# Kernel optimization log

Measured on AMD Instinct MI355X. Metric: run time of the kernel, lower is better.

## Reference

```python
import jax, jax.numpy as jnp
import numpy as np

T = 4096   # total prefill tokens
HK = 16    # local_num_k_heads
HV = 16    # local_num_v_heads
DK = 128   # head_k_dim
DV = 128   # head_v_dim
KW = 4     # linear_conv_kernel_dim
QKV = HK * DK * 2 + HV * DV  # 6144


def setup_inputs() -> dict:
    key = jax.random.key(0)
    ks = jax.random.split(key, 6)
    return {
        "mixed_qkv": jax.random.normal(ks[0], (T, QKV), jnp.float32),
        "forget_gate": jax.random.normal(ks[1], (T, HV * DK), jnp.float32),
        "beta": jax.random.normal(ks[2], (T, HV), jnp.float32),
        "conv_weights": jax.random.normal(ks[3], (QKV, KW), jnp.float32) * 0.1,
        "A_log": jax.random.normal(ks[4], (HV,), jnp.float32),
        "dt_bias": jax.random.normal(ks[5], (HV, DK), jnp.float32),
    }


def _causal_conv1d_silu(x, w):
    # x: [T, C], w: [C, K] depthwise causal conv (no bias) + SiLU, matching causal_conv1d_fn
    C = x.shape[1]
    xt = x.T[None]                       # [1, C, T]
    y = jax.lax.conv_general_dilated(
        xt, w[:, None, :], window_strides=(1,), padding=[(KW - 1, 0)],
        feature_group_count=C)           # [1, C, T]
    return jax.nn.silu(y[0].T)           # [T, C]


def _l2norm(x, eps=1e-6):
    return x * jax.lax.rsqrt(jnp.sum(x * x, axis=-1, keepdims=True) + eps)


def reference(mixed_qkv, forget_gate, beta, conv_weights, A_log, dt_bias):
    # 1) depthwise causal conv1d + silu over packed qkv
    qkv = _causal_conv1d_silu(mixed_qkv, conv_weights)
    q, k, v = jnp.split(qkv, [HK * DK, 2 * HK * DK], axis=-1)
    # use_qk_l2norm_in_kernel=True; scale=None -> DK**-0.5 applied to q
    q = _l2norm(q.reshape(T, HK, DK)) * (DK ** -0.5)
    k = _l2norm(k.reshape(T, HK, DK))
    v = v.reshape(T, HV, DV)
    # use_gate_in_kernel=True (fused_kda_gate): g = -exp(A_log) * softplus(g_raw + dt_bias)
    g = -jnp.exp(A_log)[None, :, None] * jax.nn.softplus(
        forget_gate.reshape(T, HV, DK) + dt_bias[None])      # [T, H, DK] (log-decay)
    b = jax.nn.sigmoid(beta.astype(jnp.float32))             # [T, H]

    # 2) gated delta-rule recurrence (KDA), state S: [H, DK, DV]
    def step(S, inp):
        qt, kt, vt, gt, bt = inp
        S = S * jnp.exp(gt)[:, :, None]                      # per-dim forget
        pred = jnp.einsum('hk,hkv->hv', kt, S)               # memory readout
        delta = bt[:, None] * (vt - pred)                    # delta rule
        S = S + kt[:, :, None] * delta[:, None, :]
        o = jnp.einsum('hk,hkv->hv', qt, S)
        return S, o

    S0 = jnp.zeros((HV, DK, DV), jnp.float32)  # no prior ssm cache (fresh prefill)
    _, out = jax.lax.scan(step, S0, (q, k, v, g, b))
    return out  # [T, H, DV]
```

## Files before the change

kernel.cpp:

```cpp
#include <hip/hip_runtime.h>
#include <math.h>

#define TT   4096
#define HH   16
#define DK   128
#define QKV  6144
#define NQ   2048
#define KW   4

#define CK      16
#define NCHUNK  256
#define CG      2
#define NCG     64

#define ROTADD(x, r) x += __int_as_float(__builtin_amdgcn_update_dpp( \
    0, __float_as_int(x), 0x120 + (r), 0xf, 0xf, true))

#define XHALF(x) x += __int_as_float(__builtin_amdgcn_ds_swizzle( \
    __float_as_int(x), 0x401F))

#define COMP(a, i) ((i&3)==0 ? a[(i)>>2].x : (i&3)==1 ? a[(i)>>2].y \
                  : (i&3)==2 ? a[(i)>>2].z : a[(i)>>2].w)

#define ASYNC16(glb, lds) __builtin_amdgcn_global_load_lds( \
    (const __attribute__((address_space(1))) unsigned int*)(glb), \
    (__attribute__((address_space(3))) unsigned int*)(lds), 16, 0, 0)

#define WAIT_LGKM0 do { asm volatile("s_waitcnt lgkmcnt(0)" ::: "memory"); \
    __builtin_amdgcn_sched_barrier(0); } while(0)
#define WAIT_VM(N) do { asm volatile("s_waitcnt vmcnt(" #N ")" ::: "memory"); \
    __builtin_amdgcn_sched_barrier(0); } while(0)

__global__ __launch_bounds__(256) void kda_prep(
    const float* __restrict__ x,
    const float* __restrict__ fg,
    const float* __restrict__ cw,
    const float* __restrict__ A_log,
    const float* __restrict__ dtb,
    float* __restrict__ qn,
    float* __restrict__ kn,
    float* __restrict__ gout,
    float* __restrict__ vout)
{
    __shared__ float buf[QKV];
    const int t   = blockIdx.x;
    const int tid = threadIdx.x;

    for (int c = tid; c < QKV; c += 256) {
        const float4 w = *(const float4*)(cw + (size_t)c * 4);
        float acc = 0.f;
        if (t >= 3) {
            acc = x[(size_t)(t-3)*QKV + c]*w.x + x[(size_t)(t-2)*QKV + c]*w.y
                + x[(size_t)(t-1)*QKV + c]*w.z + x[(size_t)t*QKV + c]*w.w;
        } else {
            if (t-3 >= 0) acc += x[(size_t)(t-3)*QKV + c] * w.x;
            if (t-2 >= 0) acc += x[(size_t)(t-2)*QKV + c] * w.y;
            if (t-1 >= 0) acc += x[(size_t)(t-1)*QKV + c] * w.z;
            acc += x[(size_t)t*QKV + c] * w.w;
        }
        buf[c] = acc / (1.f + expf(-acc));
    }
    __syncthreads();

    {
        const int grp = tid >> 3;
        const int l8  = tid & 7;
        const float* src = buf + grp*DK + l8*16;
        float vals[16];
        float ss = 0.f;
        #pragma unroll
        for (int i = 0; i < 16; ++i) { vals[i] = src[i]; ss += vals[i]*vals[i]; }
        ss += __shfl_xor(ss, 1);
        ss += __shfl_xor(ss, 2);
        ss += __shfl_xor(ss, 4);
        float scale = 1.0f / sqrtf(ss + 1e-6f);
        const bool isq = (grp < 16);
        if (isq) scale *= 0.08838834764831845f;
        float* dst = (isq ? (qn + (size_t)t*NQ + grp*DK)
                          : (kn + (size_t)t*NQ + (grp-16)*DK)) + l8*16;
        #pragma unroll
        for (int i = 0; i < 16; ++i) dst[i] = vals[i]*scale;
    }

    for (int c = tid; c < NQ; c += 256)
        vout[(size_t)t*NQ + c] = buf[4096 + c];

    for (int c = tid; c < NQ; c += 256) {
        const int hh = c >> 7;
        const float xx = fg[(size_t)t*NQ + c] + dtb[c];
        const float sp = fmaxf(xx, 0.f) + log1pf(expf(-fabsf(xx)));
        gout[(size_t)t*NQ + c] = -expf(A_log[hh]) * sp;
    }
}

__global__ __launch_bounds__(256) void kda_chunkpre(
    float* __restrict__ Ab, float* __restrict__ Bb, float* __restrict__ Cb,
    const float* __restrict__ beta,
    float* __restrict__ GL, float* __restrict__ Qm,
    const float* __restrict__ vin,
    float* __restrict__ vt)
{
    __shared__ float gc_s[CK][DK+1];
    __shared__ float kb[CK][DK+1];
    __shared__ float qb[CK][DK+1];
    __shared__ float ktil[CK][DK+1];
    __shared__ float vb[CK][DK+1];
    __shared__ float pmat[CK][CK];
    __shared__ float xmat[CK][CK];
    __shared__ float bvals[CK];
    const int chunk = blockIdx.x, h = blockIdx.y, tid = threadIdx.x;
    const size_t base = ((size_t)chunk*CK)*NQ + h*DK;

    if (tid < CK) {
        const float bb = beta[(size_t)(chunk*CK + tid)*HH + h];
        bvals[tid] = 1.f / (1.f + expf(-bb));
    }
    if (tid < DK) {
        const int k = tid;
        float gc[CK], kv[CK], qv[CK];
        float run = 0.f;
        #pragma unroll
        for (int j = 0; j < CK; ++j) {
            run += Cb[base + (size_t)j*NQ + k];
            gc[j] = run;
            kv[j] = Bb[base + (size_t)j*NQ + k];
            qv[j] = Ab[base + (size_t)j*NQ + k];
            gc_s[j][k] = run; kb[j][k] = kv[j]; qb[j][k] = qv[j];
        }
        const float gL = gc[CK-1];
        GL[((size_t)chunk*HH + h)*DK + k] = expf(gL);
        #pragma unroll
        for (int j = 0; j < CK; ++j) {
            const float e = expf(gc[j]);
            Ab[base + (size_t)j*NQ + k] = qv[j]*e;
            ktil[j][k] = kv[j]*e;
            Cb[base + (size_t)j*NQ + k] = kv[j]*expf(gL - gc[j]);
        }
    }
    for (int idx = tid; idx < CK*DK; idx += 256)
        vb[idx>>7][idx&127] =
            vin[(size_t)(chunk*CK + (idx>>7))*NQ + h*DK + (idx&127)];

    if (tid < CK*CK) xmat[tid>>4][tid&15] = 0.f;
    __syncthreads();

    const size_t mqbase = ((size_t)chunk*HH + h)*(CK*CK);
    if (tid < 136) {
        int j = 0, i = tid;
        while (i > j) { i -= (j+1); ++j; }
        float accp = 0.f, accq = 0.f;
        #pragma unroll 4
        for (int k = 0; k < DK; ++k) {
            const float e = __expf(gc_s[j][k] - gc_s[i][k]);
            const float kie = kb[i][k]*e;
            accq = fmaf(qb[j][k], kie, accq);
            accp = fmaf(kb[j][k], kie, accp);
        }
        Qm[mqbase + j*CK + i] = accq;
        if (j > i) pmat[j][i] = accp;
    } else {
        int a = 1, u = tid - 136;
        while (u >= a) { u -= a; ++a; }
        Qm[mqbase + u*CK + a] = 0.f;
    }
    __syncthreads();

    if (tid < CK) {
        const int i = tid;
        for (int j = i; j < CK; ++j) {
            float s = (j == i) ? 1.f : 0.f;
            for (int m = i; m < j; ++m) s -= pmat[j][m]*xmat[m][i];
            xmat[j][i] = bvals[j]*s;
        }
    }
    __syncthreads();

    for (int idx = tid; idx < CK*DK; idx += 256) {
        const int j = idx >> 7, k2 = idx & 127;
        float aE = 0.f, aV = 0.f;
        #pragma unroll
        for (int m = 0; m < CK; ++m) {
            const float xm = xmat[j][m];
            aE = fmaf(xm, ktil[m][k2], aE);
            aV = fmaf(xm, vb[m][k2], aV);
        }
        Bb[base + (size_t)j*NQ + k2] = aE;
        vt[(size_t)(chunk*CK + j)*NQ + h*DK + k2] = aV;
    }
}

__global__ __launch_bounds__(64) void kda_scan(
    const float* __restrict__ Em,
    const float* __restrict__ qS,
    const float* __restrict__ wm,
    const float* __restrict__ GL,
    const float* __restrict__ Qm,
    const float* __restrict__ vin,
    float* __restrict__ vo)
{
    __shared__ __attribute__((aligned(16))) float s_e[CK][DK];
    __shared__ __attribute__((aligned(16))) float s_q[CK][DK];
    __shared__ __attribute__((aligned(16))) float s_w[2][CK][DK];
    __shared__ __attribute__((aligned(16))) float s_g[2][DK];
    __shared__ __attribute__((aligned(16))) float s_v[CK][4];

    const int tid   = threadIdx.x;
    const int ks    = tid & 15;
    const int half  = (tid >> 4) & 1;
    const int col   = tid >> 5;
    const int h     = blockIdx.x;
    const int cgoff = blockIdx.y * CG;
    const int hoff  = h * DK;
    const int r0    = half*64 + ks*4;
    const int vcol  = (cgoff & 3) + col;

    float4 S = {0,0,0,0};
    float4 pfQ[4], Qr[4];

#define STAGE_EQV(CC) do { \
    const size_t rb_ = (size_t)(CC)*CK; \
    _Pragma("unroll") \
    for (int r_ = 0; r_ < 8; ++r_) { \
        const int f_ = tid + r_*64;                   \
        const int j_ = f_ >> 5, c4_ = f_ & 31; \
        const size_t go_ = (rb_ + j_)*NQ + hoff + c4_*4; \
        ASYNC16(Em + go_, &s_e[0][0] + f_*4); \
        ASYNC16(qS + go_, &s_q[0][0] + f_*4); \
    } \
    if (tid < 16)                                     \
        ASYNC16(vin + (rb_ + tid)*NQ + hoff + (cgoff & ~3), \
                &s_v[0][0] + tid*4); \
} while(0)

#define STAGE_WGQ(CC, BB) do { \
    const size_t rb_ = (size_t)(CC)*CK; \
    _Pragma("unroll") \
    for (int r_ = 0; r_ < 8; ++r_) { \
        const int f_ = tid + r_*64; \
        const int j_ = f_ >> 5, c4_ = f_ & 31; \
        ASYNC16(wm + (rb_ + j_)*NQ + hoff + c4_*4, &s_w[BB][0][0] + f_*4); \
    } \
    if (tid < 32)                                     \
        ASYNC16(GL + ((size_t)(CC)*HH + h)*DK + tid*4, &s_g[BB][0] + tid*4); \
    { const size_t mb_ = ((size_t)(CC)*HH + h)*256 + ks*16; \
      _Pragma("unroll") \
      for (int r_ = 0; r_ < 4; ++r_) \
          pfQ[r_] = *(const float4*)(Qm + mb_ + r_*4); } \
} while(0)

    STAGE_WGQ(0, 0);
    STAGE_EQV(0);
    WAIT_VM(0);
    #pragma unroll
    for (int r = 0; r < 4; ++r) Qr[r] = pfQ[r];

    for (int c = 0; c < NCHUNK; ++c) {
        const int p = c & 1;
        const bool more = (c + 1 < NCHUNK);
        if (more) STAGE_WGQ(c + 1, 1 - p);

        float u[CK];
        float myo0 = 0.f;
        #pragma unroll
        for (int j = 0; j < CK; ++j) {
            const float4 Ea = *(const float4*)&s_e[j][r0];
            const float4 qa = *(const float4*)&s_q[j][r0];
            float pp = Ea.x*S.x;
            pp = fmaf(Ea.y, S.y, pp); pp = fmaf(Ea.z, S.z, pp); pp = fmaf(Ea.w, S.w, pp);
            float oo = qa.x*S.x;
            oo = fmaf(qa.y, S.y, oo); oo = fmaf(qa.z, S.z, oo); oo = fmaf(qa.w, S.w, oo);
            ROTADD(pp, 8); ROTADD(pp, 4); ROTADD(pp, 2); ROTADD(pp, 1);
            ROTADD(oo, 8); ROTADD(oo, 4); ROTADD(oo, 2); ROTADD(oo, 1);
            XHALF(pp);
            XHALF(oo);
            u[j] = s_v[j][vcol] - pp;
            myo0 = (j == ks) ? oo : myo0;
        }

        WAIT_LGKM0;
        if (more) STAGE_EQV(c + 1);

        const float4 ga = *(const float4*)&s_g[p][r0];
        S.x *= ga.x; S.y *= ga.y; S.z *= ga.z; S.w *= ga.w;

        float oacc = 0.f;
        #pragma unroll
        for (int i = 0; i < CK; ++i) {
            const float ui = u[i];
            const float4 wa = *(const float4*)&s_w[p][i][r0];
            S.x = fmaf(wa.x, ui, S.x); S.y = fmaf(wa.y, ui, S.y);
            S.z = fmaf(wa.z, ui, S.z); S.w = fmaf(wa.w, ui, S.w);
            oacc = fmaf(COMP(Qr, i), ui, oacc);
        }
        if (half == 0)
            vo[((size_t)(c*CK + ks))*NQ + hoff + cgoff + col] = myo0 + oacc;

        if (more) {
            #pragma unroll
            for (int r = 0; r < 4; ++r) Qr[r] = pfQ[r];
            WAIT_VM(1);
        }
    }
#undef STAGE_EQV
#undef STAGE_WGQ
}

extern "C" void kernel_launch(void* const* d_in, const int* in_sizes, int n_in,
                              void* d_out, int out_size, void* d_ws, size_t ws_size,
                              hipStream_t stream) {
    const float* x     = (const float*)d_in[0];
    const float* fg    = (const float*)d_in[1];
    const float* beta  = (const float*)d_in[2];
    const float* cw    = (const float*)d_in[3];
    const float* A_log = (const float*)d_in[4];
    const float* dtb   = (const float*)d_in[5];
    float* out = (float*)d_out;
    float* ws  = (float*)d_ws;

    const size_t TN = (size_t)TT * NQ;
    float* A_  = ws;
    float* B_  = ws + TN;
    float* C_  = ws + 2*TN;

    float* scratch = (float*)d_in[1];
    float* GLp = scratch;
    float* Qm  = scratch + (size_t)524288;

    float* vtil = (float*)d_in[0];

    hipLaunchKernelGGL(kda_prep, dim3(TT), dim3(256), 0, stream,
                       x, fg, cw, A_log, dtb, A_, B_, C_, out);
    hipLaunchKernelGGL(kda_chunkpre, dim3(NCHUNK, HH), dim3(256), 0, stream,
                       A_, B_, C_, beta, GLp, Qm, out, vtil);
    hipLaunchKernelGGL(kda_scan, dim3(HH, NCG), dim3(64), 0, stream,
                       B_, A_, C_, GLp, Qm, vtil, out);
}
```

Before: 921.4 us.

## Give each scan thread 8 state rows and 4 value columns per block

The scan kernel is rebalanced so each lane holds two float4 slices of state (rows r and r+64) instead of one. This removes the cross-half swizzle reduction and the idle half of the lanes at output time, and each 64-lane block now covers 4 value columns instead of 2, halving the grid. The cost is more registers and LDS reads per lane on the serial chunk loop, and only half as many blocks are available to fill the GPU.

New measurement: 1.073 ms. +16.5%, slower.

```diff
diff --git a/kernel.cpp b/kernel.cpp
--- a/kernel.cpp
+++ b/kernel.cpp
@@ -10,14 +10,11 @@
 
 #define CK      16
 #define NCHUNK  256
-#define CG      2
-#define NCG     64
+#define CG      4
+#define NCG     32
 
 #define ROTADD(x, r) x += __int_as_float(__builtin_amdgcn_update_dpp( \
     0, __float_as_int(x), 0x120 + (r), 0xf, 0xf, true))
-
-#define XHALF(x) x += __int_as_float(__builtin_amdgcn_ds_swizzle( \
-    __float_as_int(x), 0x401F))
 
 #define COMP(a, i) ((i&3)==0 ? a[(i)>>2].x : (i&3)==1 ? a[(i)>>2].y \
                   : (i&3)==2 ? a[(i)>>2].z : a[(i)>>2].w)
@@ -202,19 +199,17 @@
     __shared__ __attribute__((aligned(16))) float s_q[CK][DK];
     __shared__ __attribute__((aligned(16))) float s_w[2][CK][DK];
     __shared__ __attribute__((aligned(16))) float s_g[2][DK];
-    __shared__ __attribute__((aligned(16))) float s_v[CK][4];
+    __shared__ __attribute__((aligned(16))) float s_v[CK][CG];
 
     const int tid   = threadIdx.x;
     const int ks    = tid & 15;
-    const int half  = (tid >> 4) & 1;
-    const int col   = tid >> 5;
+    const int col   = tid >> 4;
     const int h     = blockIdx.x;
     const int cgoff = blockIdx.y * CG;
     const int hoff  = h * DK;
-    const int r0    = half*64 + ks*4;
-    const int vcol  = (cgoff & 3) + col;
-
-    float4 S = {0,0,0,0};
+    const int r1 = ks*4, r2 = 64 + ks*4;
+
+    float4 S1 = {0,0,0,0}, S2 = {0,0,0,0};
     float4 pfQ[4], Qr[4];
 
 #define STAGE_EQV(CC) do { \
@@ -228,8 +223,7 @@
         ASYNC16(qS + go_, &s_q[0][0] + f_*4); \
     } \
     if (tid < 16)                                     \
-        ASYNC16(vin + (rb_ + tid)*NQ + hoff + (cgoff & ~3), \
-                &s_v[0][0] + tid*4); \
+        ASYNC16(vin + (rb_ + tid)*NQ + hoff + cgoff, &s_v[0][0] + tid*4); \
 } while(0)
 
 #define STAGE_WGQ(CC, BB) do { \
@@ -263,37 +257,47 @@
         float myo0 = 0.f;
         #pragma unroll
         for (int j = 0; j < CK; ++j) {
-            const float4 Ea = *(const float4*)&s_e[j][r0];
-            const float4 qa = *(const float4*)&s_q[j][r0];
-            float pp = Ea.x*S.x;
-            pp = fmaf(Ea.y, S.y, pp); pp = fmaf(Ea.z, S.z, pp); pp = fmaf(Ea.w, S.w, pp);
-            float oo = qa.x*S.x;
-            oo = fmaf(qa.y, S.y, oo); oo = fmaf(qa.z, S.z, oo); oo = fmaf(qa.w, S.w, oo);
+            const float4 Ea  = *(const float4*)&s_e[j][r1];
+            const float4 Eb  = *(const float4*)&s_e[j][r2];
+            const float4 qa  = *(const float4*)&s_q[j][r1];
+            const float4 qb4 = *(const float4*)&s_q[j][r2];
+            float pa = Ea.x*S1.x;
+            pa = fmaf(Ea.y, S1.y, pa); pa = fmaf(Ea.z, S1.z, pa); pa = fmaf(Ea.w, S1.w, pa);
+            float pb = Eb.x*S2.x;
+            pb = fmaf(Eb.y, S2.y, pb); pb = fmaf(Eb.z, S2.z, pb); pb = fmaf(Eb.w, S2.w, pb);
+            float pp = pa + pb;
+            float oa = qa.x*S1.x;
+            oa = fmaf(qa.y, S1.y, oa); oa = fmaf(qa.z, S1.z, oa); oa = fmaf(qa.w, S1.w, oa);
+            float ob = qb4.x*S2.x;
+            ob = fmaf(qb4.y, S2.y, ob); ob = fmaf(qb4.z, S2.z, ob); ob = fmaf(qb4.w, S2.w, ob);
+            float oo = oa + ob;
             ROTADD(pp, 8); ROTADD(pp, 4); ROTADD(pp, 2); ROTADD(pp, 1);
             ROTADD(oo, 8); ROTADD(oo, 4); ROTADD(oo, 2); ROTADD(oo, 1);
-            XHALF(pp);
-            XHALF(oo);
-            u[j] = s_v[j][vcol] - pp;
+            u[j] = s_v[j][col] - pp;
             myo0 = (j == ks) ? oo : myo0;
         }
 
         WAIT_LGKM0;
         if (more) STAGE_EQV(c + 1);
 
-        const float4 ga = *(const float4*)&s_g[p][r0];
-        S.x *= ga.x; S.y *= ga.y; S.z *= ga.z; S.w *= ga.w;
+        const float4 ga = *(const float4*)&s_g[p][r1];
+        const float4 gb = *(const float4*)&s_g[p][r2];
+        S1.x *= ga.x; S1.y *= ga.y; S1.z *= ga.z; S1.w *= ga.w;
+        S2.x *= gb.x; S2.y *= gb.y; S2.z *= gb.z; S2.w *= gb.w;
 
         float oacc = 0.f;
         #pragma unroll
         for (int i = 0; i < CK; ++i) {
             const float ui = u[i];
-            const float4 wa = *(const float4*)&s_w[p][i][r0];
-            S.x = fmaf(wa.x, ui, S.x); S.y = fmaf(wa.y, ui, S.y);
-            S.z = fmaf(wa.z, ui, S.z); S.w = fmaf(wa.w, ui, S.w);
+            const float4 wa = *(const float4*)&s_w[p][i][r1];
+            const float4 wb = *(const float4*)&s_w[p][i][r2];
+            S1.x = fmaf(wa.x, ui, S1.x); S1.y = fmaf(wa.y, ui, S1.y);
+            S1.z = fmaf(wa.z, ui, S1.z); S1.w = fmaf(wa.w, ui, S1.w);
+            S2.x = fmaf(wb.x, ui, S2.x); S2.y = fmaf(wb.y, ui, S2.y);
+            S2.z = fmaf(wb.z, ui, S2.z); S2.w = fmaf(wb.w, ui, S2.w);
             oacc = fmaf(COMP(Qr, i), ui, oacc);
         }
-        if (half == 0)
-            vo[((size_t)(c*CK + ks))*NQ + hoff + cgoff + col] = myo0 + oacc;
+        vo[((size_t)(c*CK + ks))*NQ + hoff + cgoff + col] = myo0 + oacc;
 
         if (more) {
             #pragma unroll
```

## Restructure scan LDS staging: cache E in registers, double-buffer q/v, use permlane32 swap

Applied to the files above, without the earlier changes.

Reorganizes the per-chunk staging in the recurrence scan. E rows are copied into registers so the E buffer can be refilled early. q, v and g are double-buffered and prefetched a chunk ahead, while w is single-buffered and refilled after its last use. The thread mapping swaps the half/col roles so the cross-half reduction can use permlane32_swap instead of ds_swizzle. The hand-tuned vmcnt wait counts are fragile and must match the exact number of issued async loads, and the register-cached E copy raises register pressure.

Result: slower. 961.4 us (+4.3%).

```diff
diff --git a/kernel.cpp b/kernel.cpp
--- a/kernel.cpp
+++ b/kernel.cpp
@@ -16,8 +16,11 @@
 #define ROTADD(x, r) x += __int_as_float(__builtin_amdgcn_update_dpp( \
     0, __float_as_int(x), 0x120 + (r), 0xf, 0xf, true))
 
-#define XHALF(x) x += __int_as_float(__builtin_amdgcn_ds_swizzle( \
-    __float_as_int(x), 0x401F))
+typedef int int2v __attribute__((ext_vector_type(2)));
+#define XH32(x) do { \
+    int2v r_ = __builtin_amdgcn_permlane32_swap( \
+        __float_as_int(x), __float_as_int(x), false, false); \
+    x = __int_as_float(r_[0]) + __int_as_float(r_[1]); } while(0)
 
 #define COMP(a, i) ((i&3)==0 ? a[(i)>>2].x : (i&3)==1 ? a[(i)>>2].y \
                   : (i&3)==2 ? a[(i)>>2].z : a[(i)>>2].w)
@@ -199,15 +202,15 @@
     float* __restrict__ vo)
 {
     __shared__ __attribute__((aligned(16))) float s_e[CK][DK];
-    __shared__ __attribute__((aligned(16))) float s_q[CK][DK];
-    __shared__ __attribute__((aligned(16))) float s_w[2][CK][DK];
+    __shared__ __attribute__((aligned(16))) float s_q[2][CK][DK];
+    __shared__ __attribute__((aligned(16))) float s_w[CK][DK];
     __shared__ __attribute__((aligned(16))) float s_g[2][DK];
-    __shared__ __attribute__((aligned(16))) float s_v[CK][4];
+    __shared__ __attribute__((aligned(16))) float s_v[2][CK][4];
 
     const int tid   = threadIdx.x;
     const int ks    = tid & 15;
-    const int half  = (tid >> 4) & 1;
-    const int col   = tid >> 5;
+    const int col   = (tid >> 4) & 1;
+    const int half  = tid >> 5;
     const int h     = blockIdx.x;
     const int cgoff = blockIdx.y * CG;
     const int hoff  = h * DK;
@@ -215,31 +218,19 @@
     const int vcol  = (cgoff & 3) + col;
 
     float4 S = {0,0,0,0};
-    float4 pfQ[4], Qr[4];
-
-#define STAGE_EQV(CC) do { \
+    float4 pfQ[4], Qr[4], eR[CK];
+
+#define STAGE_QVG(CC, BB) do { \
     const size_t rb_ = (size_t)(CC)*CK; \
     _Pragma("unroll") \
     for (int r_ = 0; r_ < 8; ++r_) { \
         const int f_ = tid + r_*64;                   \
         const int j_ = f_ >> 5, c4_ = f_ & 31; \
-        const size_t go_ = (rb_ + j_)*NQ + hoff + c4_*4; \
-        ASYNC16(Em + go_, &s_e[0][0] + f_*4); \
-        ASYNC16(qS + go_, &s_q[0][0] + f_*4); \
+        ASYNC16(qS + (rb_ + j_)*NQ + hoff + c4_*4, &s_q[BB][0][0] + f_*4); \
     } \
     if (tid < 16)                                     \
         ASYNC16(vin + (rb_ + tid)*NQ + hoff + (cgoff & ~3), \
-                &s_v[0][0] + tid*4); \
-} while(0)
-
-#define STAGE_WGQ(CC, BB) do { \
-    const size_t rb_ = (size_t)(CC)*CK; \
-    _Pragma("unroll") \
-    for (int r_ = 0; r_ < 8; ++r_) { \
-        const int f_ = tid + r_*64; \
-        const int j_ = f_ >> 5, c4_ = f_ & 31; \
-        ASYNC16(wm + (rb_ + j_)*NQ + hoff + c4_*4, &s_w[BB][0][0] + f_*4); \
-    } \
+                &s_v[BB][0][0] + tid*4); \
     if (tid < 32)                                     \
         ASYNC16(GL + ((size_t)(CC)*HH + h)*DK + tid*4, &s_g[BB][0] + tid*4); \
     { const size_t mb_ = ((size_t)(CC)*HH + h)*256 + ks*16; \
@@ -248,8 +239,25 @@
           pfQ[r_] = *(const float4*)(Qm + mb_ + r_*4); } \
 } while(0)
 
-    STAGE_WGQ(0, 0);
-    STAGE_EQV(0);
+#define STAGE_E(CC) do { const size_t rb_ = (size_t)(CC)*CK; \
+    _Pragma("unroll") \
+    for (int r_ = 0; r_ < 8; ++r_) { \
+        const int f_ = tid + r_*64; \
+        const int j_ = f_ >> 5, c4_ = f_ & 31; \
+        ASYNC16(Em + (rb_ + j_)*NQ + hoff + c4_*4, &s_e[0][0] + f_*4); } \
+} while(0)
+
+#define STAGE_W(CC) do { const size_t rb_ = (size_t)(CC)*CK; \
+    _Pragma("unroll") \
+    for (int r_ = 0; r_ < 8; ++r_) { \
+        const int f_ = tid + r_*64; \
+        const int j_ = f_ >> 5, c4_ = f_ & 31; \
+        ASYNC16(wm + (rb_ + j_)*NQ + hoff + c4_*4, &s_w[0][0] + f_*4); } \
+} while(0)
+
+    STAGE_QVG(0, 0);
+    STAGE_E(0);
+    STAGE_W(0);
     WAIT_VM(0);
     #pragma unroll
     for (int r = 0; r < 4; ++r) Qr[r] = pfQ[r];
@@ -257,28 +265,34 @@
     for (int c = 0; c < NCHUNK; ++c) {
         const int p = c & 1;
         const bool more = (c + 1 < NCHUNK);
-        if (more) STAGE_WGQ(c + 1, 1 - p);
+
+        if (more) STAGE_QVG(c + 1, 1 - p);
+
+        #pragma unroll
+        for (int j = 0; j < CK; ++j)
+            eR[j] = *(const float4*)&s_e[j][r0];
+        WAIT_LGKM0;
+        if (more) STAGE_E(c + 1);
 
         float u[CK];
         float myo0 = 0.f;
         #pragma unroll
         for (int j = 0; j < CK; ++j) {
-            const float4 Ea = *(const float4*)&s_e[j][r0];
-            const float4 qa = *(const float4*)&s_q[j][r0];
+            const float4 Ea = eR[j];
+            const float4 qa = *(const float4*)&s_q[p][j][r0];
             float pp = Ea.x*S.x;
             pp = fmaf(Ea.y, S.y, pp); pp = fmaf(Ea.z, S.z, pp); pp = fmaf(Ea.w, S.w, pp);
             float oo = qa.x*S.x;
             oo = fmaf(qa.y, S.y, oo); oo = fmaf(qa.z, S.z, oo); oo = fmaf(qa.w, S.w, oo);
             ROTADD(pp, 8); ROTADD(pp, 4); ROTADD(pp, 2); ROTADD(pp, 1);
             ROTADD(oo, 8); ROTADD(oo, 4); ROTADD(oo, 2); ROTADD(oo, 1);
-            XHALF(pp);
-            XHALF(oo);
-            u[j] = s_v[j][vcol] - pp;
+            XH32(pp);
+            XH32(oo);
+            u[j] = s_v[p][j][vcol] - pp;
             myo0 = (j == ks) ? oo : myo0;
         }
 
-        WAIT_LGKM0;
-        if (more) STAGE_EQV(c + 1);
+        if (more) WAIT_VM(23); else WAIT_VM(1);
 
         const float4 ga = *(const float4*)&s_g[p][r0];
         S.x *= ga.x; S.y *= ga.y; S.z *= ga.z; S.w *= ga.w;
@@ -287,22 +301,27 @@
         #pragma unroll
         for (int i = 0; i < CK; ++i) {
             const float ui = u[i];
-            const float4 wa = *(const float4*)&s_w[p][i][r0];
+            const float4 wa = *(const float4*)&s_w[i][r0];
             S.x = fmaf(wa.x, ui, S.x); S.y = fmaf(wa.y, ui, S.y);
             S.z = fmaf(wa.z, ui, S.z); S.w = fmaf(wa.w, ui, S.w);
             oacc = fmaf(COMP(Qr, i), ui, oacc);
         }
+
+        WAIT_LGKM0;
+        if (more) STAGE_W(c + 1);
+
         if (half == 0)
             vo[((size_t)(c*CK + ks))*NQ + hoff + cgoff + col] = myo0 + oacc;
 
         if (more) {
             #pragma unroll
             for (int r = 0; r < 4; ++r) Qr[r] = pfQ[r];
-            WAIT_VM(1);
-        }
-    }
-#undef STAGE_EQV
-#undef STAGE_WGQ
+            WAIT_VM(9);
+        }
+    }
+#undef STAGE_QVG
+#undef STAGE_E
+#undef STAGE_W
 }
 
 extern "C" void kernel_launch(void* const* d_in, const int* in_sizes, int n_in,
```
